# Kernel tuning notes

Hardware: AMD Instinct MI355X
Metric: run time of the kernel (lower is better)

The kernel has to match this reference:

```python
import jax, jax.numpy as jnp
import numpy as np

N = 100000
E = 3200000
DIM_IN, DIM_H, DIM_OUT = 256, 128, 64


def setup_inputs() -> dict:
    key = jax.random.key(0)
    k1, k2, k3, k4 = jax.random.split(key, 4)
    x = jax.random.normal(k1, (N, DIM_IN), dtype=jnp.float32)
    edge_index = jax.random.randint(k2, (2, E), 0, N, dtype=jnp.int32)
    # Glorot-ish init for the two GCNConv linear layers (weight + bias, PyG defaults)
    W1 = jax.random.normal(k3, (DIM_IN, DIM_H), dtype=jnp.float32) * (1.0 / np.sqrt(DIM_IN))
    b1 = jnp.zeros((DIM_H,), dtype=jnp.float32)
    W2 = jax.random.normal(k4, (DIM_H, DIM_OUT), dtype=jnp.float32) * (1.0 / np.sqrt(DIM_H))
    b2 = jnp.zeros((DIM_OUT,), dtype=jnp.float32)
    return {"x": x, "W1": W1, "b1": b1, "W2": W2, "b2": b2, "edge_index": edge_index}


def _gcn_norm(edge_index, num_nodes):
    """Add self-loops and compute symmetric D^{-1/2} A_hat D^{-1/2} edge weights."""
    loops = jnp.arange(num_nodes, dtype=edge_index.dtype)
    src = jnp.concatenate([edge_index[0], loops])
    dst = jnp.concatenate([edge_index[1], loops])
    deg = jax.ops.segment_sum(jnp.ones_like(dst, dtype=jnp.float32), dst,
                              num_segments=num_nodes)
    dinv = jnp.where(deg > 0, jax.lax.rsqrt(deg), 0.0)
    norm = dinv[src] * dinv[dst]  # [E + N]
    return src, dst, norm


def _gcn_conv(h, W, b, src, dst, norm, num_nodes):
    h = h @ W                                   # [N, F_out] linear transform first (PyG order)
    msg = norm[:, None] * h[src]                # gather + scale messages
    agg = jax.ops.segment_sum(msg, dst, num_segments=num_nodes)  # scatter-add
    return agg + b


def reference(x, W1, b1, W2, b2, edge_index):
    n = x.shape[0]
    src, dst, norm = _gcn_norm(edge_index, n)
    h = _gcn_conv(x, W1, b1, src, dst, norm, n)
    h = jax.nn.relu(h)
    h = _gcn_conv(h, W2, b2, src, dst, norm, n)
    return jax.nn.log_softmax(h, axis=1)
```

## Files before the change

### kernel.cpp

```cpp
#include <hip/hip_runtime.h>
#include <hip/hip_bf16.h>

#define WAVE 64
typedef unsigned int uint32;
typedef __attribute__((ext_vector_type(8))) short bf16x8;
typedef __attribute__((ext_vector_type(4))) float f32x4;

__device__ inline float bf16lo(uint32 u) { return __uint_as_float(u << 16); }
__device__ inline float bf16hi(uint32 u) { return __uint_as_float(u & 0xffff0000u); }
__device__ inline uint32 f2bf(float f) {
    union { float f; uint32 u; } a; a.f = f;
    uint32 u = a.u;
    u += 0x7fffu + ((u >> 16) & 1u);
    return u >> 16;
}
__device__ inline uint32 packbf(float lo, float hi) { return f2bf(lo) | (f2bf(hi) << 16); }
__device__ inline short f2bfs(float f) { return (short)f2bf(f); }

__global__ void convert_w_kernel(const float* __restrict__ W1, const float* __restrict__ W2,
                                 uint32* __restrict__ w1f, uint32* __restrict__ w2f,
                                 int* __restrict__ gcnt) {
    int tid = blockIdx.x * blockDim.x + threadIdx.x;
    if (tid < 256) gcnt[tid] = 0;
    if (tid < 16384) {
        int w = tid & 3, l = (tid >> 2) & 63, c = (tid >> 8) & 7, kc = tid >> 11;
        int q = l & 15, g = l >> 4;
        int k0 = kc * 32 + g * 8 + 2 * w;
        int n = c * 16 + q;
        w1f[tid] = packbf(W1[k0 * 128 + n], W1[(k0 + 1) * 128 + n]);
    } else if (tid < 16384 + 4096) {
        int t = tid - 16384;
        int w = t & 3, l = (t >> 2) & 63, c = (t >> 8) & 3, kc = t >> 10;
        int q = l & 15, g = l >> 4;
        int k0 = kc * 32 + g * 8 + 2 * w;
        int n = c * 16 + q;
        w2f[t] = packbf(W2[k0 * 64 + n], W2[(k0 + 1) * 64 + n]);
    }
}

#define BIN_TB 1024
#define BIN_EPB 4096
__global__ __launch_bounds__(BIN_TB) void binsort_kernel(const int* __restrict__ src,
                                                         const int* __restrict__ dst,
                                                         int* __restrict__ gcnt,
                                                         uint32* __restrict__ pairs,
                                                         int E, int CAP) {
    __shared__ int hist[256];
    __shared__ int scan[256];
    __shared__ int lstart[256];
    __shared__ int gbase[256];
    __shared__ int lcur[256];
    __shared__ uint32 sp[BIN_EPB];
    __shared__ unsigned char sb[BIN_EPB];
    int tid = threadIdx.x;
    int base = blockIdx.x * BIN_EPB;
    if (tid < 256) hist[tid] = 0;
    __syncthreads();
    int s[4], b[4];
    uint32 pk[4];
    bool v[4];
#pragma unroll
    for (int j = 0; j < 4; ++j) {
        int e = base + tid + j * BIN_TB;
        v[j] = e < E;
        if (v[j]) {
            s[j] = src[e];
            int d = dst[e];
            b[j] = d >> 9;
            pk[j] = (uint32)s[j] | ((uint32)(d & 511) << 17);
            atomicAdd(&hist[b[j]], 1);
        }
    }
    __syncthreads();
    if (tid < 256) scan[tid] = hist[tid];
    __syncthreads();
#pragma unroll
    for (int o = 1; o < 256; o <<= 1) {
        int t = 0;
        if (tid < 256 && tid >= o) t = scan[tid - o];
        __syncthreads();
        if (tid < 256) scan[tid] += t;
        __syncthreads();
    }
    if (tid < 256) {
        int st = scan[tid] - hist[tid];
        lstart[tid] = st;
        lcur[tid] = st;
        gbase[tid] = (hist[tid] > 0) ? (tid * CAP + atomicAdd(&gcnt[tid], hist[tid])) : 0;
    }
    __syncthreads();
#pragma unroll
    for (int j = 0; j < 4; ++j) {
        if (v[j]) {
            int p = atomicAdd(&lcur[b[j]], 1);
            sp[p] = pk[j];
            sb[p] = (unsigned char)b[j];
        }
    }
    __syncthreads();
    int total = scan[255];
    for (int i = tid; i < total; i += BIN_TB) {
        int bb = sb[i];
        pairs[gbase[bb] + (i - lstart[bb])] = sp[i];
    }
}

__global__ __launch_bounds__(512) void bucket_csr_kernel(const uint32* __restrict__ pairs,
                                                         const int* __restrict__ gcnt,
                                                         int* __restrict__ sorted,
                                                         int* __restrict__ rowstart,
                                                         int* __restrict__ rowend,
                                                         float* __restrict__ dinv,
                                                         int N, int CAP) {
    __shared__ int cnt[512];
    __shared__ int incl[512];
    __shared__ int cursor[512];
    extern __shared__ uint32 ssorted[];
    int b = blockIdx.x;
    int tid = threadIdx.x;
    int ne = gcnt[b];
    if (ne > CAP) ne = CAP;
    const uint32* P = pairs + (size_t)b * CAP;
    cnt[tid] = 0;
    __syncthreads();
    for (int i = tid; i < ne; i += 512) atomicAdd(&cnt[P[i] >> 17], 1);
    __syncthreads();
    int v = cnt[tid];
    incl[tid] = v;
    __syncthreads();
#pragma unroll
    for (int o = 1; o < 512; o <<= 1) {
        int t = (tid >= o) ? incl[tid - o] : 0;
        __syncthreads();
        incl[tid] += t;
        __syncthreads();
    }
    int gbase = b * CAP;
    int node = b * 512 + tid;
    if (node < N) {
        rowstart[node] = gbase + incl[tid] - v;
        rowend[node] = gbase + incl[tid];
        dinv[node] = rsqrtf(1.0f + (float)v);
    }
    cursor[tid] = incl[tid] - v;
    __syncthreads();
    for (int i = tid; i < ne; i += 512) {
        uint32 p = P[i];
        int ln = p >> 17;
        int r = atomicAdd(&cursor[ln], 1);
        ssorted[r] = p & 0x1FFFFu;
    }
    __syncthreads();
    for (int i = tid; i < ne; i += 512) sorted[gbase + i] = (int)ssorted[i];
}

__global__ __launch_bounds__(256) void gemm1_mfma(const float* __restrict__ x,
                                                  const uint32* __restrict__ w1f,
                                                  const float* __restrict__ dinv,
                                                  uint32* __restrict__ hout,
                                                  int N) {
    const bf16x8* Bp = (const bf16x8*)w1f;
    int l = threadIdx.x & 63, w = threadIdx.x >> 6;
    int q = l & 15, g = l >> 4;
    int R = blockIdx.x * 128 + w * 32;
    f32x4 acc[2][8];
#pragma unroll
    for (int rt = 0; rt < 2; ++rt)
#pragma unroll
        for (int c = 0; c < 8; ++c) acc[rt][c] = (f32x4){0.f, 0.f, 0.f, 0.f};

#pragma unroll
    for (int kc = 0; kc < 8; ++kc) {
        bf16x8 b[8];
#pragma unroll
        for (int c = 0; c < 8; ++c) b[c] = Bp[(kc * 8 + c) * 64 + l];
#pragma unroll
        for (int rt = 0; rt < 2; ++rt) {
            int row = R + rt * 16 + q;
            row = row < N ? row : N - 1;
            const float* xr = x + (size_t)row * 256 + kc * 32 + g * 8;
            float4 xa = *(const float4*)xr;
            float4 xb = *(const float4*)(xr + 4);
            bf16x8 a;
            a[0] = f2bfs(xa.x); a[1] = f2bfs(xa.y); a[2] = f2bfs(xa.z); a[3] = f2bfs(xa.w);
            a[4] = f2bfs(xb.x); a[5] = f2bfs(xb.y); a[6] = f2bfs(xb.z); a[7] = f2bfs(xb.w);
#pragma unroll
            for (int c = 0; c < 8; ++c)
                acc[rt][c] = __builtin_amdgcn_mfma_f32_16x16x32_bf16(a, b[c], acc[rt][c], 0, 0, 0);
        }
    }
#pragma unroll
    for (int rt = 0; rt < 2; ++rt)
#pragma unroll
        for (int r = 0; r < 4; ++r) {
            int grow = R + rt * 16 + 4 * g + r;
            if (grow < N) {
                float wd = dinv[grow];
                uint32* orow = hout + (size_t)grow * 64;
#pragma unroll
                for (int c = 0; c < 4; ++c)
                    orow[c * 16 + q] = packbf(acc[rt][c][r] * wd, acc[rt][c + 4][r] * wd);
            }
        }
}

__global__ __launch_bounds__(256) void agg1_kernel(const uint32* __restrict__ h,
                                                   const float* __restrict__ dinv,
                                                   const int* __restrict__ srt,
                                                   const int* __restrict__ rowstart,
                                                   const int* __restrict__ rowend,
                                                   const float* __restrict__ bias,
                                                   uint32* __restrict__ out,
                                                   int n) {
    int wid = (int)(((long)blockIdx.x * blockDim.x + threadIdx.x) >> 6);
    int lane = threadIdx.x & 63;
    if (wid >= n) return;
    const uint2* h2 = (const uint2*)h;
    int q = lane & 31;
    int half = lane >> 5;
    int start = rowstart[wid];
    int end = rowend[wid];
    float a0 = 0.f, a1 = 0.f, a2 = 0.f, a3 = 0.f;
    if (half == 0) {
        uint2 us = h2[(size_t)wid * 32 + q];
        a0 = bf16lo(us.x); a1 = bf16hi(us.x);
        a2 = bf16lo(us.y); a3 = bf16hi(us.y);
    }
    int e = start + half;
    for (; e + 6 < end; e += 8) {
        int s0 = srt[e], s1 = srt[e + 2], s2 = srt[e + 4], s3 = srt[e + 6];
        uint2 u0 = h2[(size_t)s0 * 32 + q];
        uint2 u1 = h2[(size_t)s1 * 32 + q];
        uint2 u2 = h2[(size_t)s2 * 32 + q];
        uint2 u3 = h2[(size_t)s3 * 32 + q];
        a0 += bf16lo(u0.x); a1 += bf16hi(u0.x); a2 += bf16lo(u0.y); a3 += bf16hi(u0.y);
        a0 += bf16lo(u1.x); a1 += bf16hi(u1.x); a2 += bf16lo(u1.y); a3 += bf16hi(u1.y);
        a0 += bf16lo(u2.x); a1 += bf16hi(u2.x); a2 += bf16lo(u2.y); a3 += bf16hi(u2.y);
        a0 += bf16lo(u3.x); a1 += bf16hi(u3.x); a2 += bf16lo(u3.y); a3 += bf16hi(u3.y);
    }
    for (; e < end; e += 2) {
        uint2 u = h2[(size_t)srt[e] * 32 + q];
        a0 += bf16lo(u.x); a1 += bf16hi(u.x);
        a2 += bf16lo(u.y); a3 += bf16hi(u.y);
    }
    a0 += __shfl_xor(a0, 32, WAVE);
    a1 += __shfl_xor(a1, 32, WAVE);
    a2 += __shfl_xor(a2, 32, WAVE);
    a3 += __shfl_xor(a3, 32, WAVE);
    float wd = dinv[wid];
    float2 blo = ((const float2*)bias)[q];
    float2 bhi = ((const float2*)bias)[q + 32];
    float v0 = fmaxf(fmaf(wd, a0, blo.x), 0.f);
    float v2 = fmaxf(fmaf(wd, a2, blo.y), 0.f);
    float v1 = fmaxf(fmaf(wd, a1, bhi.x), 0.f);
    float v3 = fmaxf(fmaf(wd, a3, bhi.y), 0.f);
    uint32* orow = out + (size_t)wid * 64;
    if (half == 0) orow[q] = packbf(v0, v2);
    else           orow[q + 32] = packbf(v1, v3);
}

__global__ __launch_bounds__(256) void gemm2_mfma(const uint32* __restrict__ hin,
                                                  const uint32* __restrict__ w2f,
                                                  const float* __restrict__ dinv,
                                                  uint32* __restrict__ hout,
                                                  int N) {
    const bf16x8* Bp = (const bf16x8*)w2f;
    const short* hs = (const short*)hin;
    int l = threadIdx.x & 63, w = threadIdx.x >> 6;
    int q = l & 15, g = l >> 4;
    int R = blockIdx.x * 128 + w * 32;
    f32x4 acc[2][4];
#pragma unroll
    for (int rt = 0; rt < 2; ++rt)
#pragma unroll
        for (int c = 0; c < 4; ++c) acc[rt][c] = (f32x4){0.f, 0.f, 0.f, 0.f};

#pragma unroll
    for (int kc = 0; kc < 4; ++kc) {
        bf16x8 b[4];
#pragma unroll
        for (int c = 0; c < 4; ++c) b[c] = Bp[(kc * 4 + c) * 64 + l];
#pragma unroll
        for (int rt = 0; rt < 2; ++rt) {
            int row = R + rt * 16 + q;
            row = row < N ? row : N - 1;
            bf16x8 a = *(const bf16x8*)(hs + (size_t)row * 128 + kc * 32 + g * 8);
#pragma unroll
            for (int c = 0; c < 4; ++c)
                acc[rt][c] = __builtin_amdgcn_mfma_f32_16x16x32_bf16(a, b[c], acc[rt][c], 0, 0, 0);
        }
    }
#pragma unroll
    for (int rt = 0; rt < 2; ++rt)
#pragma unroll
        for (int r = 0; r < 4; ++r) {
            int grow = R + rt * 16 + 4 * g + r;
            if (grow < N) {
                float wd = dinv[grow];
                uint32* orow = hout + (size_t)grow * 32;
#pragma unroll
                for (int c = 0; c < 2; ++c)
                    orow[c * 16 + q] = packbf(acc[rt][c][r] * wd, acc[rt][c + 2][r] * wd);
            }
        }
}

__global__ __launch_bounds__(256) void agg2_ls_kernel(const uint32* __restrict__ h,
                                                      const float* __restrict__ dinv,
                                                      const int* __restrict__ srt,
                                                      const int* __restrict__ rowstart,
                                                      const int* __restrict__ rowend,
                                                      const float* __restrict__ bias,
                                                      float* __restrict__ out, int n) {
    int wid = (int)(((long)blockIdx.x * blockDim.x + threadIdx.x) >> 6);
    int lane = threadIdx.x & 63;
    if (wid >= n) return;
    const uint2* h2 = (const uint2*)h;
    int q = lane & 15;
    int quad = lane >> 4;
    int start = rowstart[wid];
    int end = rowend[wid];
    float a0 = 0.f, a1 = 0.f, a2 = 0.f, a3 = 0.f;
    if (quad == 0) {
        uint2 us = h2[(size_t)wid * 16 + q];
        a0 = bf16lo(us.x); a1 = bf16hi(us.x);
        a2 = bf16lo(us.y); a3 = bf16hi(us.y);
    }
    int e = start + quad;
    for (; e + 12 < end; e += 16) {
        int s0 = srt[e], s1 = srt[e + 4], s2 = srt[e + 8], s3 = srt[e + 12];
        uint2 u0 = h2[(size_t)s0 * 16 + q];
        uint2 u1 = h2[(size_t)s1 * 16 + q];
        uint2 u2 = h2[(size_t)s2 * 16 + q];
        uint2 u3 = h2[(size_t)s3 * 16 + q];
        a0 += bf16lo(u0.x); a1 += bf16hi(u0.x); a2 += bf16lo(u0.y); a3 += bf16hi(u0.y);
        a0 += bf16lo(u1.x); a1 += bf16hi(u1.x); a2 += bf16lo(u1.y); a3 += bf16hi(u1.y);
        a0 += bf16lo(u2.x); a1 += bf16hi(u2.x); a2 += bf16lo(u2.y); a3 += bf16hi(u2.y);
        a0 += bf16lo(u3.x); a1 += bf16hi(u3.x); a2 += bf16lo(u3.y); a3 += bf16hi(u3.y);
    }
    for (; e < end; e += 4) {
        uint2 u = h2[(size_t)srt[e] * 16 + q];
        a0 += bf16lo(u.x); a1 += bf16hi(u.x);
        a2 += bf16lo(u.y); a3 += bf16hi(u.y);
    }
#pragma unroll
    for (int o = 16; o <= 32; o <<= 1) {
        a0 += __shfl_xor(a0, o, WAVE);
        a1 += __shfl_xor(a1, o, WAVE);
        a2 += __shfl_xor(a2, o, WAVE);
        a3 += __shfl_xor(a3, o, WAVE);
    }
    float wd = dinv[wid];
    float2 blo = ((const float2*)bias)[q];
    float2 bhi = ((const float2*)bias)[q + 16];
    float v0 = fmaf(wd, a0, blo.x);
    float v2 = fmaf(wd, a2, blo.y);
    float v1 = fmaf(wd, a1, bhi.x);
    float v3 = fmaf(wd, a3, bhi.y);
    float m = fmaxf(fmaxf(v0, v1), fmaxf(v2, v3));
#pragma unroll
    for (int o = 8; o; o >>= 1) m = fmaxf(m, __shfl_xor(m, o, WAVE));
    float s = __expf(v0 - m) + __expf(v1 - m) + __expf(v2 - m) + __expf(v3 - m);
#pragma unroll
    for (int o = 8; o; o >>= 1) s += __shfl_xor(s, o, WAVE);
    float lg = __logf(s) + m;
    if (quad == 0)
        *(float2*)&out[(size_t)wid * 64 + 2 * q] = make_float2(v0 - lg, v2 - lg);
    else if (quad == 1)
        *(float2*)&out[(size_t)wid * 64 + 32 + 2 * q] = make_float2(v1 - lg, v3 - lg);
}

extern "C" void kernel_launch(void* const* d_in, const int* in_sizes, int n_in,
                              void* d_out, int out_size, void* d_ws, size_t ws_size,
                              hipStream_t stream) {
    const float* x  = (const float*)d_in[0];
    const float* W1 = (const float*)d_in[1];
    const float* b1 = (const float*)d_in[2];
    const float* W2 = (const float*)d_in[3];
    const float* b2 = (const float*)d_in[4];
    const int* edge = (const int*)d_in[5];

    const int N = in_sizes[0] / 256;
    const int E = in_sizes[5] / 2;
    const int* src = edge;
    const int* dst = edge + E;

    const int NBUCK = (N + 511) >> 9;
    int mean = E / NBUCK;
    int CAP = mean + (int)(8.5 * __builtin_sqrt((double)mean)) + 32;
    CAP = (CAP + 63) & ~63;
    if (CAP > 36864) CAP = 36864;

    int*    gcnt     = (int*)d_ws;
    uint32* w1f      = (uint32*)(gcnt + 256);
    uint32* w2f      = w1f + 16384;
    float*  dinv     = (float*)(w2f + 4096);
    int*    rowstart = (int*)(dinv + N);
    int*    rowend   = rowstart + N;
    int*    sorted   = rowend + N;
    uint32* h1s      = (uint32*)(sorted + (size_t)NBUCK * CAP);
    uint32* h2s      = h1s + (size_t)N * 64;
    uint32* agg1bf   = h2s + (size_t)N * 32;
    uint32* pairs    = agg1bf;
    float*  outp     = (float*)d_out;

    const int TB = 256;

    convert_w_kernel<<<80, TB, 0, stream>>>(W1, W2, w1f, w2f, gcnt);

    binsort_kernel<<<(E + BIN_EPB - 1) / BIN_EPB, BIN_TB, 0, stream>>>(src, dst, gcnt, pairs, E, CAP);
    bucket_csr_kernel<<<NBUCK, 512, (size_t)CAP * 4, stream>>>(pairs, gcnt, sorted, rowstart, rowend, dinv, N, CAP);

    gemm1_mfma<<<(N + 127) / 128, TB, 0, stream>>>(x, w1f, dinv, h1s, N);

    agg1_kernel<<<(N * 64 + TB - 1) / TB, TB, 0, stream>>>(h1s, dinv, sorted, rowstart, rowend, b1, agg1bf, N);

    gemm2_mfma<<<(N + 127) / 128, TB, 0, stream>>>(agg1bf, w2f, dinv, h2s, N);

    agg2_ls_kernel<<<(N * 64 + TB - 1) / TB, TB, 0, stream>>>(h2s, dinv, sorted, rowstart, rowend, b2, outp, N);
}
```

Measured before the change: 268.8 us.

## Split layer-1 features into two planes and gather 16-byte rows per edge

The first-layer transformed features are written as two separate 64-byte-per-node planes, and aggregation runs as two passes, one per plane. This keeps each gathered working set half the size so it is more likely to stay in cache. Both aggregation kernels now load 16 bytes per lane with 8 lanes per row and 8 edges in flight per wave. The cost is reading the CSR index arrays twice, an extra launch, and deeper shuffle reductions.

```diff
diff --git a/kernel.cpp b/kernel.cpp
--- a/kernel.cpp
+++ b/kernel.cpp
@@ -157,7 +157,8 @@
 __global__ __launch_bounds__(256) void gemm1_mfma(const float* __restrict__ x,
                                                   const uint32* __restrict__ w1f,
                                                   const float* __restrict__ dinv,
-                                                  uint32* __restrict__ hout,
+                                                  uint32* __restrict__ h1a,
+                                                  uint32* __restrict__ h1b,
                                                   int N) {
     const bf16x8* Bp = (const bf16x8*)w1f;
     int l = threadIdx.x & 63, w = threadIdx.x >> 6;
@@ -196,67 +197,87 @@
             int grow = R + rt * 16 + 4 * g + r;
             if (grow < N) {
                 float wd = dinv[grow];
-                uint32* orow = hout + (size_t)grow * 64;
-#pragma unroll
-                for (int c = 0; c < 4; ++c)
-                    orow[c * 16 + q] = packbf(acc[rt][c][r] * wd, acc[rt][c + 4][r] * wd);
+#pragma unroll
+                for (int c = 0; c < 4; ++c) {
+                    uint32 val = packbf(acc[rt][c][r] * wd, acc[rt][c + 4][r] * wd);
+                    uint32* pl = (c < 2) ? h1a : h1b;
+                    pl[(size_t)grow * 32 + (c & 1) * 16 + q] = val;
+                }
             }
         }
 }
 
-__global__ __launch_bounds__(256) void agg1_kernel(const uint32* __restrict__ h,
-                                                   const float* __restrict__ dinv,
-                                                   const int* __restrict__ srt,
-                                                   const int* __restrict__ rowstart,
-                                                   const int* __restrict__ rowend,
-                                                   const float* __restrict__ bias,
-                                                   uint32* __restrict__ out,
-                                                   int n) {
+__global__ __launch_bounds__(256) void agg1_plane_kernel(const uint32* __restrict__ hp,
+                                                         const float* __restrict__ dinv,
+                                                         const int* __restrict__ srt,
+                                                         const int* __restrict__ rowstart,
+                                                         const int* __restrict__ rowend,
+                                                         const float* __restrict__ bias,
+                                                         uint32* __restrict__ out,
+                                                         int n, int plane) {
     int wid = (int)(((long)blockIdx.x * blockDim.x + threadIdx.x) >> 6);
     int lane = threadIdx.x & 63;
     if (wid >= n) return;
-    const uint2* h2 = (const uint2*)h;
-    int q = lane & 31;
-    int half = lane >> 5;
+    const uint4* h4 = (const uint4*)hp;
+    int q = lane & 7;
+    int g = lane >> 3;
     int start = rowstart[wid];
     int end = rowend[wid];
-    float a0 = 0.f, a1 = 0.f, a2 = 0.f, a3 = 0.f;
-    if (half == 0) {
-        uint2 us = h2[(size_t)wid * 32 + q];
-        a0 = bf16lo(us.x); a1 = bf16hi(us.x);
-        a2 = bf16lo(us.y); a3 = bf16hi(us.y);
-    }
-    int e = start + half;
-    for (; e + 6 < end; e += 8) {
-        int s0 = srt[e], s1 = srt[e + 2], s2 = srt[e + 4], s3 = srt[e + 6];
-        uint2 u0 = h2[(size_t)s0 * 32 + q];
-        uint2 u1 = h2[(size_t)s1 * 32 + q];
-        uint2 u2 = h2[(size_t)s2 * 32 + q];
-        uint2 u3 = h2[(size_t)s3 * 32 + q];
-        a0 += bf16lo(u0.x); a1 += bf16hi(u0.x); a2 += bf16lo(u0.y); a3 += bf16hi(u0.y);
-        a0 += bf16lo(u1.x); a1 += bf16hi(u1.x); a2 += bf16lo(u1.y); a3 += bf16hi(u1.y);
-        a0 += bf16lo(u2.x); a1 += bf16hi(u2.x); a2 += bf16lo(u2.y); a3 += bf16hi(u2.y);
-        a0 += bf16lo(u3.x); a1 += bf16hi(u3.x); a2 += bf16lo(u3.y); a3 += bf16hi(u3.y);
-    }
-    for (; e < end; e += 2) {
-        uint2 u = h2[(size_t)srt[e] * 32 + q];
-        a0 += bf16lo(u.x); a1 += bf16hi(u.x);
-        a2 += bf16lo(u.y); a3 += bf16hi(u.y);
-    }
-    a0 += __shfl_xor(a0, 32, WAVE);
-    a1 += __shfl_xor(a1, 32, WAVE);
-    a2 += __shfl_xor(a2, 32, WAVE);
-    a3 += __shfl_xor(a3, 32, WAVE);
+    float aL0 = 0.f, aL1 = 0.f, aL2 = 0.f, aL3 = 0.f;
+    float aH0 = 0.f, aH1 = 0.f, aH2 = 0.f, aH3 = 0.f;
+    if (g == 0) {
+        uint4 u = h4[(size_t)wid * 8 + q];
+        aL0 = bf16lo(u.x); aH0 = bf16hi(u.x);
+        aL1 = bf16lo(u.y); aH1 = bf16hi(u.y);
+        aL2 = bf16lo(u.z); aH2 = bf16hi(u.z);
+        aL3 = bf16lo(u.w); aH3 = bf16hi(u.w);
+    }
+    int e = start + g;
+    for (; e + 24 < end; e += 32) {
+        int s0 = srt[e], s1 = srt[e + 8], s2 = srt[e + 16], s3 = srt[e + 24];
+        uint4 u0 = h4[(size_t)s0 * 8 + q];
+        uint4 u1 = h4[(size_t)s1 * 8 + q];
+        uint4 u2 = h4[(size_t)s2 * 8 + q];
+        uint4 u3 = h4[(size_t)s3 * 8 + q];
+        aL0 += bf16lo(u0.x); aH0 += bf16hi(u0.x); aL1 += bf16lo(u0.y); aH1 += bf16hi(u0.y);
+        aL2 += bf16lo(u0.z); aH2 += bf16hi(u0.z); aL3 += bf16lo(u0.w); aH3 += bf16hi(u0.w);
+        aL0 += bf16lo(u1.x); aH0 += bf16hi(u1.x); aL1 += bf16lo(u1.y); aH1 += bf16hi(u1.y);
+        aL2 += bf16lo(u1.z); aH2 += bf16hi(u1.z); aL3 += bf16lo(u1.w); aH3 += bf16hi(u1.w);
+        aL0 += bf16lo(u2.x); aH0 += bf16hi(u2.x); aL1 += bf16lo(u2.y); aH1 += bf16hi(u2.y);
+        aL2 += bf16lo(u2.z); aH2 += bf16hi(u2.z); aL3 += bf16lo(u2.w); aH3 += bf16hi(u2.w);
+        aL0 += bf16lo(u3.x); aH0 += bf16hi(u3.x); aL1 += bf16lo(u3.y); aH1 += bf16hi(u3.y);
+        aL2 += bf16lo(u3.z); aH2 += bf16hi(u3.z); aL3 += bf16lo(u3.w); aH3 += bf16hi(u3.w);
+    }
+    for (; e < end; e += 8) {
+        uint4 u = h4[(size_t)srt[e] * 8 + q];
+        aL0 += bf16lo(u.x); aH0 += bf16hi(u.x); aL1 += bf16lo(u.y); aH1 += bf16hi(u.y);
+        aL2 += bf16lo(u.z); aH2 += bf16hi(u.z); aL3 += bf16lo(u.w); aH3 += bf16hi(u.w);
+    }
+#pragma unroll
+    for (int o = 8; o <= 32; o <<= 1) {
+        aL0 += __shfl_xor(aL0, o, WAVE); aL1 += __shfl_xor(aL1, o, WAVE);
+        aL2 += __shfl_xor(aL2, o, WAVE); aL3 += __shfl_xor(aL3, o, WAVE);
+        aH0 += __shfl_xor(aH0, o, WAVE); aH1 += __shfl_xor(aH1, o, WAVE);
+        aH2 += __shfl_xor(aH2, o, WAVE); aH3 += __shfl_xor(aH3, o, WAVE);
+    }
     float wd = dinv[wid];
-    float2 blo = ((const float2*)bias)[q];
-    float2 bhi = ((const float2*)bias)[q + 32];
-    float v0 = fmaxf(fmaf(wd, a0, blo.x), 0.f);
-    float v2 = fmaxf(fmaf(wd, a2, blo.y), 0.f);
-    float v1 = fmaxf(fmaf(wd, a1, bhi.x), 0.f);
-    float v3 = fmaxf(fmaf(wd, a3, bhi.y), 0.f);
-    uint32* orow = out + (size_t)wid * 64;
-    if (half == 0) orow[q] = packbf(v0, v2);
-    else           orow[q + 32] = packbf(v1, v3);
+    if (g == 0) {
+        int f = plane * 32 + 4 * q;
+        float4 b = *(const float4*)(bias + f);
+        float v0 = fmaxf(fmaf(wd, aL0, b.x), 0.f);
+        float v1 = fmaxf(fmaf(wd, aL1, b.y), 0.f);
+        float v2 = fmaxf(fmaf(wd, aL2, b.z), 0.f);
+        float v3 = fmaxf(fmaf(wd, aL3, b.w), 0.f);
+        ((uint2*)(out + (size_t)wid * 64))[plane * 8 + q] = make_uint2(packbf(v0, v1), packbf(v2, v3));
+    } else if (g == 1) {
+        int f = plane * 32 + 4 * q;
+        float4 b = *(const float4*)(bias + 64 + f);
+        float v0 = fmaxf(fmaf(wd, aH0, b.x), 0.f);
+        float v1 = fmaxf(fmaf(wd, aH1, b.y), 0.f);
+        float v2 = fmaxf(fmaf(wd, aH2, b.z), 0.f);
+        float v3 = fmaxf(fmaf(wd, aH3, b.w), 0.f);
+        ((uint2*)(out + (size_t)wid * 64))[16 + plane * 8 + q] = make_uint2(packbf(v0, v1), packbf(v2, v3));
+    }
 }
 
 __global__ __launch_bounds__(256) void gemm2_mfma(const uint32* __restrict__ hin,
@@ -315,59 +336,68 @@
     int wid = (int)(((long)blockIdx.x * blockDim.x + threadIdx.x) >> 6);
     int lane = threadIdx.x & 63;
     if (wid >= n) return;
-    const uint2* h2 = (const uint2*)h;
-    int q = lane & 15;
-    int quad = lane >> 4;
+    const uint4* h4 = (const uint4*)h;
+    int q = lane & 7;
+    int g = lane >> 3;
     int start = rowstart[wid];
     int end = rowend[wid];
-    float a0 = 0.f, a1 = 0.f, a2 = 0.f, a3 = 0.f;
-    if (quad == 0) {
-        uint2 us = h2[(size_t)wid * 16 + q];
-        a0 = bf16lo(us.x); a1 = bf16hi(us.x);
-        a2 = bf16lo(us.y); a3 = bf16hi(us.y);
-    }
-    int e = start + quad;
-    for (; e + 12 < end; e += 16) {
-        int s0 = srt[e], s1 = srt[e + 4], s2 = srt[e + 8], s3 = srt[e + 12];
-        uint2 u0 = h2[(size_t)s0 * 16 + q];
-        uint2 u1 = h2[(size_t)s1 * 16 + q];
-        uint2 u2 = h2[(size_t)s2 * 16 + q];
-        uint2 u3 = h2[(size_t)s3 * 16 + q];
-        a0 += bf16lo(u0.x); a1 += bf16hi(u0.x); a2 += bf16lo(u0.y); a3 += bf16hi(u0.y);
-        a0 += bf16lo(u1.x); a1 += bf16hi(u1.x); a2 += bf16lo(u1.y); a3 += bf16hi(u1.y);
-        a0 += bf16lo(u2.x); a1 += bf16hi(u2.x); a2 += bf16lo(u2.y); a3 += bf16hi(u2.y);
-        a0 += bf16lo(u3.x); a1 += bf16hi(u3.x); a2 += bf16lo(u3.y); a3 += bf16hi(u3.y);
-    }
-    for (; e < end; e += 4) {
-        uint2 u = h2[(size_t)srt[e] * 16 + q];
-        a0 += bf16lo(u.x); a1 += bf16hi(u.x);
-        a2 += bf16lo(u.y); a3 += bf16hi(u.y);
-    }
-#pragma unroll
-    for (int o = 16; o <= 32; o <<= 1) {
-        a0 += __shfl_xor(a0, o, WAVE);
-        a1 += __shfl_xor(a1, o, WAVE);
-        a2 += __shfl_xor(a2, o, WAVE);
-        a3 += __shfl_xor(a3, o, WAVE);
+    float aL0 = 0.f, aL1 = 0.f, aL2 = 0.f, aL3 = 0.f;
+    float aH0 = 0.f, aH1 = 0.f, aH2 = 0.f, aH3 = 0.f;
+    if (g == 0) {
+        uint4 u = h4[(size_t)wid * 8 + q];
+        aL0 = bf16lo(u.x); aH0 = bf16hi(u.x);
+        aL1 = bf16lo(u.y); aH1 = bf16hi(u.y);
+        aL2 = bf16lo(u.z); aH2 = bf16hi(u.z);
+        aL3 = bf16lo(u.w); aH3 = bf16hi(u.w);
+    }
+    int e = start + g;
+    for (; e + 24 < end; e += 32) {
+        int s0 = srt[e], s1 = srt[e + 8], s2 = srt[e + 16], s3 = srt[e + 24];
+        uint4 u0 = h4[(size_t)s0 * 8 + q];
+        uint4 u1 = h4[(size_t)s1 * 8 + q];
+        uint4 u2 = h4[(size_t)s2 * 8 + q];
+        uint4 u3 = h4[(size_t)s3 * 8 + q];
+        aL0 += bf16lo(u0.x); aH0 += bf16hi(u0.x); aL1 += bf16lo(u0.y); aH1 += bf16hi(u0.y);
+        aL2 += bf16lo(u0.z); aH2 += bf16hi(u0.z); aL3 += bf16lo(u0.w); aH3 += bf16hi(u0.w);
+        aL0 += bf16lo(u1.x); aH0 += bf16hi(u1.x); aL1 += bf16lo(u1.y); aH1 += bf16hi(u1.y);
+        aL2 += bf16lo(u1.z); aH2 += bf16hi(u1.z); aL3 += bf16lo(u1.w); aH3 += bf16hi(u1.w);
+        aL0 += bf16lo(u2.x); aH0 += bf16hi(u2.x); aL1 += bf16lo(u2.y); aH1 += bf16hi(u2.y);
+        aL2 += bf16lo(u2.z); aH2 += bf16hi(u2.z); aL3 += bf16lo(u2.w); aH3 += bf16hi(u2.w);
+        aL0 += bf16lo(u3.x); aH0 += bf16hi(u3.x); aL1 += bf16lo(u3.y); aH1 += bf16hi(u3.y);
+        aL2 += bf16lo(u3.z); aH2 += bf16hi(u3.z); aL3 += bf16lo(u3.w); aH3 += bf16hi(u3.w);
+    }
+    for (; e < end; e += 8) {
+        uint4 u = h4[(size_t)srt[e] * 8 + q];
+        aL0 += bf16lo(u.x); aH0 += bf16hi(u.x); aL1 += bf16lo(u.y); aH1 += bf16hi(u.y);
+        aL2 += bf16lo(u.z); aH2 += bf16hi(u.z); aL3 += bf16lo(u.w); aH3 += bf16hi(u.w);
+    }
+#pragma unroll
+    for (int o = 8; o <= 32; o <<= 1) {
+        aL0 += __shfl_xor(aL0, o, WAVE); aL1 += __shfl_xor(aL1, o, WAVE);
+        aL2 += __shfl_xor(aL2, o, WAVE); aL3 += __shfl_xor(aL3, o, WAVE);
+        aH0 += __shfl_xor(aH0, o, WAVE); aH1 += __shfl_xor(aH1, o, WAVE);
+        aH2 += __shfl_xor(aH2, o, WAVE); aH3 += __shfl_xor(aH3, o, WAVE);
     }
     float wd = dinv[wid];
-    float2 blo = ((const float2*)bias)[q];
-    float2 bhi = ((const float2*)bias)[q + 16];
-    float v0 = fmaf(wd, a0, blo.x);
-    float v2 = fmaf(wd, a2, blo.y);
-    float v1 = fmaf(wd, a1, bhi.x);
-    float v3 = fmaf(wd, a3, bhi.y);
-    float m = fmaxf(fmaxf(v0, v1), fmaxf(v2, v3));
-#pragma unroll
-    for (int o = 8; o; o >>= 1) m = fmaxf(m, __shfl_xor(m, o, WAVE));
-    float s = __expf(v0 - m) + __expf(v1 - m) + __expf(v2 - m) + __expf(v3 - m);
-#pragma unroll
-    for (int o = 8; o; o >>= 1) s += __shfl_xor(s, o, WAVE);
+    float4 bL = *(const float4*)(bias + 4 * q);
+    float4 bH = *(const float4*)(bias + 32 + 4 * q);
+    float vL0 = fmaf(wd, aL0, bL.x), vL1 = fmaf(wd, aL1, bL.y);
+    float vL2 = fmaf(wd, aL2, bL.z), vL3 = fmaf(wd, aL3, bL.w);
+    float vH0 = fmaf(wd, aH0, bH.x), vH1 = fmaf(wd, aH1, bH.y);
+    float vH2 = fmaf(wd, aH2, bH.z), vH3 = fmaf(wd, aH3, bH.w);
+    float m = fmaxf(fmaxf(fmaxf(vL0, vL1), fmaxf(vL2, vL3)),
+                    fmaxf(fmaxf(vH0, vH1), fmaxf(vH2, vH3)));
+#pragma unroll
+    for (int o = 1; o <= 4; o <<= 1) m = fmaxf(m, __shfl_xor(m, o, WAVE));
+    float s = __expf(vL0 - m) + __expf(vL1 - m) + __expf(vL2 - m) + __expf(vL3 - m) +
+              __expf(vH0 - m) + __expf(vH1 - m) + __expf(vH2 - m) + __expf(vH3 - m);
+#pragma unroll
+    for (int o = 1; o <= 4; o <<= 1) s += __shfl_xor(s, o, WAVE);
     float lg = __logf(s) + m;
-    if (quad == 0)
-        *(float2*)&out[(size_t)wid * 64 + 2 * q] = make_float2(v0 - lg, v2 - lg);
-    else if (quad == 1)
-        *(float2*)&out[(size_t)wid * 64 + 32 + 2 * q] = make_float2(v1 - lg, v3 - lg);
+    if (g == 0)
+        *(float4*)&out[(size_t)wid * 64 + 4 * q] = make_float4(vL0 - lg, vL1 - lg, vL2 - lg, vL3 - lg);
+    else if (g == 1)
+        *(float4*)&out[(size_t)wid * 64 + 32 + 4 * q] = make_float4(vH0 - lg, vH1 - lg, vH2 - lg, vH3 - lg);
 }
 
 extern "C" void kernel_launch(void* const* d_in, const int* in_sizes, int n_in,
@@ -398,8 +428,9 @@
     int*    rowstart = (int*)(dinv + N);
     int*    rowend   = rowstart + N;
     int*    sorted   = rowend + N;
-    uint32* h1s      = (uint32*)(sorted + (size_t)NBUCK * CAP);
-    uint32* h2s      = h1s + (size_t)N * 64;
+    uint32* h1a      = (uint32*)(sorted + (size_t)NBUCK * CAP);
+    uint32* h1b      = h1a + (size_t)N * 32;
+    uint32* h2s      = h1b + (size_t)N * 32;
     uint32* agg1bf   = h2s + (size_t)N * 32;
     uint32* pairs    = agg1bf;
     float*  outp     = (float*)d_out;
@@ -411,9 +442,10 @@
     binsort_kernel<<<(E + BIN_EPB - 1) / BIN_EPB, BIN_TB, 0, stream>>>(src, dst, gcnt, pairs, E, CAP);
     bucket_csr_kernel<<<NBUCK, 512, (size_t)CAP * 4, stream>>>(pairs, gcnt, sorted, rowstart, rowend, dinv, N, CAP);
 
-    gemm1_mfma<<<(N + 127) / 128, TB, 0, stream>>>(x, w1f, dinv, h1s, N);
-
-    agg1_kernel<<<(N * 64 + TB - 1) / TB, TB, 0, stream>>>(h1s, dinv, sorted, rowstart, rowend, b1, agg1bf, N);
+    gemm1_mfma<<<(N + 127) / 128, TB, 0, stream>>>(x, w1f, dinv, h1a, h1b, N);
+
+    agg1_plane_kernel<<<(N * 64 + TB - 1) / TB, TB, 0, stream>>>(h1a, dinv, sorted, rowstart, rowend, b1, agg1bf, N, 0);
+    agg1_plane_kernel<<<(N * 64 + TB - 1) / TB, TB, 0, stream>>>(h1b, dinv, sorted, rowstart, rowend, b1, agg1bf, N, 1);
 
     gemm2_mfma<<<(N + 127) / 128, TB, 0, stream>>>(agg1bf, w2f, dinv, h2s, N);
 
```

New measurement: 280.0 us. +4.2%, slower.
